# Optimization experiments

Measured on AMD Instinct MI355X. Metric: run time of the kernel, lower is better.

Reference implementation:

```python
import jax, jax.numpy as jnp
import numpy as np

N, NFEAT, NFEAT_EXT, NHID, NCLASS, NHEADS = 8192, 512, 128, 256, 10, 8


def setup_inputs() -> dict:
    key = jax.random.key(0)
    ks = jax.random.split(key, 12)
    s = lambda fan_in: 1.0 / np.sqrt(fan_in)
    return {
        "x": jax.random.normal(ks[0], (N, NFEAT), jnp.float32),
        "adj": jax.random.uniform(ks[1], (N, N), jnp.float32) / N,  # row-stochastic-ish normalized adjacency
        "sub_fea": jax.random.normal(ks[2], (1, NFEAT_EXT), jnp.float32),
        # GraphConvolution 1: nfeat -> nhid
        "gc1_W": jax.random.normal(ks[3], (NFEAT, NHID), jnp.float32) * s(NFEAT),
        "gc1_b": jnp.zeros((NHID,), jnp.float32),
        # GraphConvolution 2: nhid -> 2*nhid
        "gc2_W": jax.random.normal(ks[4], (NHID, 2 * NHID), jnp.float32) * s(NHID),
        "gc2_b": jnp.zeros((2 * NHID,), jnp.float32),
        # fc1: nfeat_ext -> nhid
        "fc1_W": jax.random.normal(ks[5], (NFEAT_EXT, NHID), jnp.float32) * s(NFEAT_EXT),
        "fc1_b": jnp.zeros((NHID,), jnp.float32),
        # AttentionLayer(3*nhid, nclass, nheads): per-head projection + softmax head gating
        "att_W": jax.random.normal(ks[6], (NHEADS, 3 * NHID, NCLASS), jnp.float32) * s(3 * NHID),
        "att_a": jax.random.normal(ks[7], (NHEADS, 3 * NHID), jnp.float32) * s(3 * NHID),
        "att_b": jnp.zeros((NCLASS,), jnp.float32),
    }


def reference(x, adj, sub_fea, gc1_W, gc1_b, gc2_W, gc2_b, fc1_W, fc1_b, att_W, att_a, att_b):
    # GCN layer 1: adj @ (x @ W) + b, then ReLU
    h = jax.nn.relu(adj @ (x @ gc1_W) + gc1_b)            # [N, nhid]
    # GCN layer 2
    h = jax.nn.relu(adj @ (h @ gc2_W) + gc2_b)            # [N, 2*nhid]
    # global_mean_pool(batch=None): mean over all nodes -> single graph vector
    g = jax.nn.selu(jnp.mean(h, axis=0, keepdims=True))    # [1, 2*nhid]
    # dropout is identity in eval mode
    x_ext = sub_fea @ fc1_W + fc1_b                        # [1, nhid]
    z = jnp.concatenate([g, x_ext], axis=1)                # [1, 3*nhid]
    # multi-head attention fusion: softmax over head scores gating per-head projections
    scores = jnp.einsum("bi,hi->bh", z, att_a)            # [1, nheads]
    alpha = jax.nn.softmax(scores, axis=1)
    head_out = jnp.einsum("bi,hio->bho", z, att_W)        # [1, nheads, nclass]
    out = jnp.einsum("bh,bho->bo", alpha, head_out) + att_b  # [1, nclass]
    return jax.nn.log_softmax(out, axis=1)
```

## Files before the change

### kernel.cpp

```cpp
#include <hip/hip_runtime.h>

typedef __attribute__((ext_vector_type(8))) short short8;
typedef __attribute__((ext_vector_type(4))) float floatx4;
typedef unsigned short ushort_t;
typedef unsigned int u32;

__device__ __forceinline__ ushort_t f2bf(float x) {
  union { float f; unsigned int u; } v; v.f = x;
  unsigned int u = v.u;
  return (ushort_t)((u + 0x7FFFu + ((u >> 16) & 1u)) >> 16);
}
__device__ __forceinline__ unsigned int pk2(float a, float b) {
  return (unsigned int)f2bf(a) | ((unsigned int)f2bf(b) << 16);
}
__device__ __forceinline__ float bf_lo(u32 u) {
  union { u32 u; float f; } v; v.u = u << 16; return v.f;
}
__device__ __forceinline__ float bf_hi(u32 u) {
  union { u32 u; float f; } v; v.u = u & 0xFFFF0000u; return v.f;
}
__device__ __forceinline__ void gl_lds16(const void* g, void* l) {
  __builtin_amdgcn_global_load_lds(
      (const __attribute__((address_space(1))) u32*)g,
      (__attribute__((address_space(3))) u32*)l, 16, 0, 0);
}


__global__ void prep_t(const float* __restrict__ W1, const float* __restrict__ W2,
                       ushort_t* __restrict__ W1T, ushort_t* __restrict__ W2T) {
  int idx = blockIdx.x * 256 + threadIdx.x;
  int m = idx >> 9, k = idx & 511;
  W1T[((m >> 7) * 64 + (k >> 3)) * 1024 + (m & 127) * 8 + (k & 7)] = f2bf(W1[k * 256 + m]);
  int m2 = idx >> 8, k2 = idx & 255;
  W2T[((m2 >> 7) * 32 + (k2 >> 3)) * 1024 + (m2 & 127) * 8 + (k2 & 7)] = f2bf(W2[k2 * 512 + m2]);
}

__global__ __launch_bounds__(256) void tile_cvt(const float* __restrict__ src,
                                                ushort_t* __restrict__ dst, const int K) {
  __shared__ __align__(16) ushort_t ls[33024];
  const int t = threadIdx.x;
  const int rb = blockIdx.y, cb = blockIdx.x;
  const long sbase = (long)rb * 128 * K + cb * 256;
#pragma unroll 4
  for (int i = 0; i < 32; ++i) {
    int flat = i * 256 + t;
    int row = flat >> 6, kq = flat & 63;
    float4 v = *(const float4*)(src + sbase + (long)row * K + kq * 4);
    *(uint2*)(ls + ((kq >> 1) * 129 + row) * 8 + (kq & 1) * 4) =
        make_uint2(pk2(v.x, v.y), pk2(v.z, v.w));
  }
  __syncthreads();
  ushort_t* ob = dst + ((long)rb * (K >> 3) + cb * 32) * 1024;
  const uint4* lv = (const uint4*)ls;
  uint4* ov = (uint4*)ob;
#pragma unroll 4
  for (int i = 0; i < 16; ++i) {
    int o = i * 256 + t;
    ov[o] = lv[(o >> 7) * 129 + (o & 127)];
  }
}

template<int MT, int NT, int EPI>
__global__ __launch_bounds__(256, 2)
void gemm_t(const ushort_t* __restrict__ A, const ushort_t* __restrict__ B,
            const float* __restrict__ bias, float* __restrict__ Cf,
            float* __restrict__ gacc, const int K, const int N) {
  constexpr int MF = MT / 32, NF = NT / 32;
  constexpr int nA = MT / 64, nB = NT / 64;
  __shared__ __align__(16) ushort_t Als[2][MT * 32];
  __shared__ __align__(16) ushort_t Bls[2][NT * 32];

  const int t = threadIdx.x;
  const int lane = t & 63, w = t >> 6;
  const int wm = w >> 1, wn = w & 1;
  const int ml = lane & 15, quad = lane >> 4;
  const int m0 = blockIdx.y * MT, n0 = blockIdx.x * NT;
  const int Kper = K / gridDim.z, kbeg = blockIdx.z * Kper;

  const char* Ag = (const char*)(A + ((long)((m0 / MT) * (K >> 3) + (kbeg >> 3)) * MT) * 8);
  const char* Bg = (const char*)(B + ((long)((n0 / NT) * (K >> 3) + (kbeg >> 3)) * NT) * 8);

  floatx4 acc[MF][NF] = {};
  const int iters = Kper >> 5;

#pragma unroll
  for (int c = 0; c < nA; ++c)
    gl_lds16(Ag + c * 4096 + t * 16, (char*)Als[0] + c * 4096 + t * 16);
#pragma unroll
  for (int c = 0; c < nB; ++c)
    gl_lds16(Bg + c * 4096 + t * 16, (char*)Bls[0] + c * 4096 + t * 16);
  Ag += MT * 64; Bg += NT * 64;

  for (int it = 0; it < iters; ++it) {
    const int cur = it & 1, nxt = cur ^ 1;
    __syncthreads();
    if (it + 1 < iters) {
#pragma unroll
      for (int c = 0; c < nA; ++c)
        gl_lds16(Ag + c * 4096 + t * 16, (char*)Als[nxt] + c * 4096 + t * 16);
#pragma unroll
      for (int c = 0; c < nB; ++c)
        gl_lds16(Bg + c * 4096 + t * 16, (char*)Bls[nxt] + c * 4096 + t * 16);
      Ag += MT * 64; Bg += NT * 64;
    }

    short8 av[MF], bv[NF];
#pragma unroll
    for (int f = 0; f < MF; ++f)
      av[f] = *(const short8*)(&Als[cur][0] + (quad * MT + wm * (MT / 2) + f * 16 + ml) * 8);
#pragma unroll
    for (int f = 0; f < NF; ++f)
      bv[f] = *(const short8*)(&Bls[cur][0] + (quad * NT + wn * (NT / 2) + f * 16 + ml) * 8);
#pragma unroll
    for (int fm = 0; fm < MF; ++fm)
#pragma unroll
      for (int fn = 0; fn < NF; ++fn)
        acc[fm][fn] = __builtin_amdgcn_mfma_f32_16x16x32_bf16(av[fm], bv[fn], acc[fm][fn], 0, 0, 0);
  }

  if constexpr (EPI == 2) {
#pragma unroll
    for (int fm = 0; fm < MF; ++fm) {
      int rowb = m0 + wm * (MT / 2) + fm * 16 + quad * 4;
#pragma unroll
      for (int r = 0; r < 4; ++r) {
        float bb = bias[rowb + r];
        float s = 0.f;
#pragma unroll
        for (int fn = 0; fn < NF; ++fn)
          s += fmaxf(acc[fm][fn][r] + bb, 0.f);
        s += __shfl_xor(s, 1);
        s += __shfl_xor(s, 2);
        s += __shfl_xor(s, 4);
        s += __shfl_xor(s, 8);
        if (ml == 0) atomicAdd(gacc + rowb + r, s);
      }
    }
  } else if constexpr (EPI == 3) {
    const int tv = (NT == 256) ? blockIdx.y : blockIdx.x;
    u32* base = (u32*)Cf + ((long)blockIdx.z * 64 + tv) * (MF * NF * 8 * 64)
                + (w * MF * NF * 2) * 64 + lane;
#pragma unroll
    for (int fm = 0; fm < MF; ++fm)
#pragma unroll
      for (int fn = 0; fn < NF; ++fn)
#pragma unroll
        for (int rp = 0; rp < 2; ++rp)
          base[((fm * NF + fn) * 2 + rp) * 64] =
              pk2(acc[fm][fn][2 * rp], acc[fm][fn][2 * rp + 1]);
  } else {
    ushort_t* C = (ushort_t*)Cf;
#pragma unroll
    for (int fm = 0; fm < MF; ++fm)
#pragma unroll
      for (int fn = 0; fn < NF; ++fn) {
        int gm = m0 + wm * (MT / 2) + fm * 16 + quad * 4;
        int gn = n0 + wn * (NT / 2) + fn * 16 + ml;
        long ob = (long)(gn >> 3) * 2048 + (gn & 7);
#pragma unroll
        for (int r = 0; r < 4; ++r)
          C[ob + (long)(gm + r) * 8] = f2bf(acc[fm][fn][r]);
      }
  }
}

__global__ void reduce_L1b(const u32* __restrict__ p, ushort_t* __restrict__ h1T,
                           const float* __restrict__ bias) {
  long i = (long)blockIdx.x * 256 + threadIdx.x;
  long o = i * 4;
  int row = (int)((o >> 3) & 255);
  int k0 = (int)((o >> 11) << 3) + (int)(o & 7);
  int tx = k0 >> 7, c0 = k0 & 127;
  int wm = row >> 7, fm = (row >> 4) & 7, quad = (row >> 2) & 3, r = row & 3;
  int wn = c0 >> 6, fn = (c0 >> 4) & 3, ml = c0 & 15;
  int slot = (((wm * 2 + wn) * 8 + fm) * 4 + fn) * 2 + (r >> 1);
  const u32* src = p + (long)tx * 16384 + slot * 64 + quad * 16 + ml;
  const bool hi = r & 1;
  float s0 = 0, s1 = 0, s2 = 0, s3 = 0;
  for (int z = 0; z < 8; ++z) {
    uint4 v = *(const uint4*)(src + (long)z * 1048576);
    if (hi) { s0 += bf_hi(v.x); s1 += bf_hi(v.y); s2 += bf_hi(v.z); s3 += bf_hi(v.w); }
    else    { s0 += bf_lo(v.x); s1 += bf_lo(v.y); s2 += bf_lo(v.z); s3 += bf_lo(v.w); }
  }
  float bb = bias[row];
  s0 = fmaxf(s0 + bb, 0.f); s1 = fmaxf(s1 + bb, 0.f);
  s2 = fmaxf(s2 + bb, 0.f); s3 = fmaxf(s3 + bb, 0.f);
  *(uint2*)(h1T + o) = make_uint2(pk2(s0, s1), pk2(s2, s3));
}

__global__ void reduce_L2a(const u32* __restrict__ p, ushort_t* __restrict__ P_t) {
  long i = (long)blockIdx.x * 256 + threadIdx.x;
  long o = i * 4;
  int row = (int)((o >> 3) & 127);
  int kc = (int)((o >> 10) & 31);
  int ty = (int)(o >> 15);
  int k0 = kc * 8 + (int)(o & 7);
  int wm = row >> 6, fm = (row >> 4) & 3, quad = (row >> 2) & 3, r = row & 3;
  int wn = k0 >> 7, fn = (k0 >> 4) & 7, ml = k0 & 15;
  int slot = (((wm * 2 + wn) * 4 + fm) * 8 + fn) * 2 + (r >> 1);
  const u32* src = p + (long)ty * 16384 + slot * 64 + quad * 16 + ml;
  const bool hi = r & 1;
  float s0 = 0, s1 = 0, s2 = 0, s3 = 0;
  for (int z = 0; z < 8; ++z) {
    uint4 v = *(const uint4*)(src + (long)z * 1048576);
    if (hi) { s0 += bf_hi(v.x); s1 += bf_hi(v.y); s2 += bf_hi(v.z); s3 += bf_hi(v.w); }
    else    { s0 += bf_lo(v.x); s1 += bf_lo(v.y); s2 += bf_lo(v.z); s3 += bf_lo(v.w); }
  }
  *(uint2*)(P_t + o) = make_uint2(pk2(s0, s1), pk2(s2, s3));
}

__global__ void tail_kernel(const float* __restrict__ gacc, const float* __restrict__ sub_fea,
                            const float* __restrict__ fc1_W, const float* __restrict__ fc1_b,
                            const float* __restrict__ att_W, const float* __restrict__ att_a,
                            const float* __restrict__ att_b, float* __restrict__ out) {
  __shared__ float z[768];
  __shared__ float sc[8];
  __shared__ float alpha[8];
  __shared__ float outsh[10];
  const int t = threadIdx.x;

  for (int j = t; j < 512; j += 256) {
    float x = gacc[j] * (1.0f / 8192.0f);
    const float scale = 1.0507009873554805f, al = 1.6732632423543772f;
    z[j] = x > 0.f ? scale * x : scale * al * (expf(x) - 1.0f);
  }
  {
    float a = fc1_b[t];
    for (int i = 0; i < 128; ++i) a += sub_fea[i] * fc1_W[i * 256 + t];
    z[512 + t] = a;
  }
  if (t < 10) outsh[t] = 0.f;
  __syncthreads();

  {
    int h = t >> 5, ln = t & 31;
    float p = 0.f;
    for (int i = ln; i < 768; i += 32) p += z[i] * att_a[h * 768 + i];
    for (int m = 16; m; m >>= 1) p += __shfl_down(p, m, 32);
    if (ln == 0) sc[h] = p;
  }
  __syncthreads();
  if (t == 0) {
    float mx = sc[0];
    for (int h = 1; h < 8; ++h) mx = fmaxf(mx, sc[h]);
    float s = 0.f, e[8];
    for (int h = 0; h < 8; ++h) { e[h] = expf(sc[h] - mx); s += e[h]; }
    for (int h = 0; h < 8; ++h) alpha[h] = e[h] / s;
  }
  __syncthreads();

  float p[10];
#pragma unroll
  for (int o = 0; o < 10; ++o) p[o] = 0.f;
  for (int i = t; i < 768; i += 256) {
    float zi = z[i];
    for (int h = 0; h < 8; ++h) {
      float za = zi * alpha[h];
      const float* wp = att_W + (h * 768 + i) * 10;
#pragma unroll
      for (int o = 0; o < 10; ++o) p[o] += za * wp[o];
    }
  }
#pragma unroll
  for (int o = 0; o < 10; ++o) atomicAdd(&outsh[o], p[o]);
  __syncthreads();
  if (t == 0) {
    float v[10], mx = -1e30f;
    for (int o = 0; o < 10; ++o) { v[o] = outsh[o] + att_b[o]; mx = fmaxf(mx, v[o]); }
    float s = 0.f;
    for (int o = 0; o < 10; ++o) s += expf(v[o] - mx);
    float lse = logf(s) + mx;
    for (int o = 0; o < 10; ++o) out[o] = v[o] - lse;
  }
}

extern "C" void kernel_launch(void* const* d_in, const int* in_sizes, int n_in,
                              void* d_out, int out_size, void* d_ws, size_t ws_size,
                              hipStream_t stream) {
  const float* x       = (const float*)d_in[0];
  const float* adj     = (const float*)d_in[1];
  const float* sub_fea = (const float*)d_in[2];
  const float* gc1_W   = (const float*)d_in[3];
  const float* gc1_b   = (const float*)d_in[4];
  const float* gc2_W   = (const float*)d_in[5];
  const float* gc2_b   = (const float*)d_in[6];
  const float* fc1_W   = (const float*)d_in[7];
  const float* fc1_b   = (const float*)d_in[8];
  const float* att_W   = (const float*)d_in[9];
  const float* att_a   = (const float*)d_in[10];
  const float* att_b   = (const float*)d_in[11];
  float* out = (float*)d_out;

  const size_t MB = 1u << 20;
  char* ws = (char*)d_ws;
  size_t off = 0;
  ushort_t* adjT = (ushort_t*)(ws + off); off += 128 * MB;
  ushort_t* xT   = (ushort_t*)(ws + off); off += 8 * MB;
  ushort_t* t1T  = (ushort_t*)(ws + off); off += 4 * MB;
  ushort_t* h1T  = (ushort_t*)(ws + off); off += 4 * MB;
  ushort_t* P_t  = (ushort_t*)(ws + off); off += 4 * MB;
  u32*      part = (u32*)     (ws + off); off += 32 * MB;
  ushort_t* W1T  = (ushort_t*)(ws + off); off += 262144;
  ushort_t* W2T  = (ushort_t*)(ws + off); off += 262144;
  float*    gacc = (float*)   (ws + off);

  hipMemsetAsync(gacc, 0, 512 * sizeof(float), stream);
  prep_t<<<512, 256, 0, stream>>>(gc1_W, gc2_W, W1T, W2T);

  tile_cvt<<<dim3(32, 64), 256, 0, stream>>>(adj, adjT, 8192);
  tile_cvt<<<dim3(2, 64), 256, 0, stream>>>(x, xT, 512);

  gemm_t<128, 128, 4><<<dim3(64, 2, 1), 256, 0, stream>>>(
      W1T, xT, nullptr, (float*)t1T, nullptr, 512, 8192);

  gemm_t<256, 128, 3><<<dim3(64, 1, 8), 256, 0, stream>>>(
      t1T, adjT, nullptr, (float*)part, nullptr, 8192, 8192);
  reduce_L1b<<<2048, 256, 0, stream>>>(part, h1T, gc1_b);

  gemm_t<128, 256, 3><<<dim3(1, 64, 8), 256, 0, stream>>>(
      adjT, h1T, nullptr, (float*)part, nullptr, 8192, 256);
  reduce_L2a<<<2048, 256, 0, stream>>>(part, P_t);

  gemm_t<128, 128, 2><<<dim3(64, 4, 1), 256, 0, stream>>>(
      W2T, P_t, gc2_b, nullptr, gacc, 256, 8192);

  tail_kernel<<<1, 256, 0, stream>>>(gacc, sub_fea, fc1_W, fc1_b, att_W, att_a, att_b, out);
}
```

Baseline: 615.6 us.

## Switch adjacency GEMMs to FP8 MFMA with scaled FP8 operands

Converts the adjacency matrix to FP8 (scaled by N) instead of bf16, and stores the t1 and h1 intermediates as FP8 with compensating scales. The two large adjacency GEMMs then use a new FP8 MFMA kernel. This halves the bytes of the dominant adjacency read and conversion write and uses the higher-throughput FP8 matrix path. The cost is lower precision from FP8 rounding, plus scale factors that have to be undone in the reduce kernels.

Result: faster. 588.4 us (-4.4%).

```diff
diff --git a/kernel.cpp b/kernel.cpp
--- a/kernel.cpp
+++ b/kernel.cpp
@@ -4,6 +4,7 @@
 typedef __attribute__((ext_vector_type(4))) float floatx4;
 typedef unsigned short ushort_t;
 typedef unsigned int u32;
+typedef unsigned char u8;
 
 __device__ __forceinline__ ushort_t f2bf(float x) {
   union { float f; unsigned int u; } v; v.f = x;
@@ -18,6 +19,14 @@
 }
 __device__ __forceinline__ float bf_hi(u32 u) {
   union { u32 u; float f; } v; v.u = u & 0xFFFF0000u; return v.f;
+}
+__device__ __forceinline__ u32 pk4_fp8(float a, float b, float c, float d) {
+  int r = __builtin_amdgcn_cvt_pk_fp8_f32(a, b, 0, false);
+  r = __builtin_amdgcn_cvt_pk_fp8_f32(c, d, r, true);
+  return (u32)r;
+}
+__device__ __forceinline__ u8 f2fp8(float a) {
+  return (u8)(__builtin_amdgcn_cvt_pk_fp8_f32(a, 0.f, 0, false) & 0xFF);
 }
 __device__ __forceinline__ void gl_lds16(const void* g, void* l) {
   __builtin_amdgcn_global_load_lds(
@@ -60,10 +69,35 @@
   }
 }
 
+__global__ __launch_bounds__(256) void tile_cvt8(const float* __restrict__ src,
+                                                 u8* __restrict__ dst) {
+  __shared__ __align__(16) u32 lsu[32 * 260];
+  const int t = threadIdx.x;
+  const int rb = blockIdx.y, cb = blockIdx.x;
+  const long sbase = (long)rb * 128 * 8192 + cb * 256;
+#pragma unroll 4
+  for (int i = 0; i < 32; ++i) {
+    int flat = i * 256 + t;
+    int row = flat >> 6, kq = flat & 63;
+    float4 v = *(const float4*)(src + sbase + (long)row * 8192 + kq * 4);
+    lsu[(kq >> 1) * 260 + row * 2 + (kq & 1)] =
+        pk4_fp8(v.x * 8192.f, v.y * 8192.f, v.z * 8192.f, v.w * 8192.f);
+  }
+  __syncthreads();
+  u8* ob = dst + ((long)rb * 1024 + cb * 32) * 1024;
+  const uint4* lv = (const uint4*)lsu;
+  uint4* ov = (uint4*)ob;
+#pragma unroll 4
+  for (int i = 0; i < 8; ++i) {
+    int o = i * 256 + t;
+    ov[o] = lv[(o >> 6) * 65 + (o & 63)];
+  }
+}
+
 template<int MT, int NT, int EPI>
 __global__ __launch_bounds__(256, 2)
 void gemm_t(const ushort_t* __restrict__ A, const ushort_t* __restrict__ B,
-            const float* __restrict__ bias, float* __restrict__ Cf,
+            const float* __restrict__ bias, void* __restrict__ Cv,
             float* __restrict__ gacc, const int K, const int N) {
   constexpr int MF = MT / 32, NF = NT / 32;
   constexpr int nA = MT / 64, nB = NT / 64;
@@ -103,7 +137,6 @@
         gl_lds16(Bg + c * 4096 + t * 16, (char*)Bls[nxt] + c * 4096 + t * 16);
       Ag += MT * 64; Bg += NT * 64;
     }
-
     short8 av[MF], bv[NF];
 #pragma unroll
     for (int f = 0; f < MF; ++f)
@@ -136,20 +169,8 @@
         if (ml == 0) atomicAdd(gacc + rowb + r, s);
       }
     }
-  } else if constexpr (EPI == 3) {
-    const int tv = (NT == 256) ? blockIdx.y : blockIdx.x;
-    u32* base = (u32*)Cf + ((long)blockIdx.z * 64 + tv) * (MF * NF * 8 * 64)
-                + (w * MF * NF * 2) * 64 + lane;
-#pragma unroll
-    for (int fm = 0; fm < MF; ++fm)
-#pragma unroll
-      for (int fn = 0; fn < NF; ++fn)
-#pragma unroll
-        for (int rp = 0; rp < 2; ++rp)
-          base[((fm * NF + fn) * 2 + rp) * 64] =
-              pk2(acc[fm][fn][2 * rp], acc[fm][fn][2 * rp + 1]);
   } else {
-    ushort_t* C = (ushort_t*)Cf;
+    u8* C8 = (u8*)Cv;
 #pragma unroll
     for (int fm = 0; fm < MF; ++fm)
 #pragma unroll
@@ -159,12 +180,81 @@
         long ob = (long)(gn >> 3) * 2048 + (gn & 7);
 #pragma unroll
         for (int r = 0; r < 4; ++r)
-          C[ob + (long)(gm + r) * 8] = f2bf(acc[fm][fn][r]);
+          C8[ob + (long)(gm + r) * 8] = f2fp8(acc[fm][fn][r]);
       }
   }
 }
 
-__global__ void reduce_L1b(const u32* __restrict__ p, ushort_t* __restrict__ h1T,
+template<int MT, int NT>
+__global__ __launch_bounds__(256, 2)
+void gemm8_t(const u8* __restrict__ A, const u8* __restrict__ B,
+             u32* __restrict__ Cp, const int K) {
+  constexpr int MF = MT / 32, NF = NT / 32;
+  constexpr int nA = MT / 128, nB = NT / 128;
+  __shared__ __align__(16) u8 Als[2][MT * 32];
+  __shared__ __align__(16) u8 Bls[2][NT * 32];
+
+  const int t = threadIdx.x;
+  const int lane = t & 63, w = t >> 6;
+  const int wm = w >> 1, wn = w & 1;
+  const int ml = lane & 15, quad = lane >> 4;
+  const int m0 = blockIdx.y * MT, n0 = blockIdx.x * NT;
+  const int Kper = K / gridDim.z, kbeg = blockIdx.z * Kper;
+
+  const u8* Ag = A + ((long)((m0 / MT) * (K >> 3) + (kbeg >> 3))) * (MT * 8);
+  const u8* Bg = B + ((long)((n0 / NT) * (K >> 3) + (kbeg >> 3))) * (NT * 8);
+
+  floatx4 acc[MF][NF] = {};
+  const int iters = Kper >> 5;
+
+#pragma unroll
+  for (int c = 0; c < nA; ++c)
+    gl_lds16(Ag + c * 4096 + t * 16, &Als[0][0] + c * 4096 + t * 16);
+#pragma unroll
+  for (int c = 0; c < nB; ++c)
+    gl_lds16(Bg + c * 4096 + t * 16, &Bls[0][0] + c * 4096 + t * 16);
+  Ag += MT * 32; Bg += NT * 32;
+
+  for (int it = 0; it < iters; ++it) {
+    const int cur = it & 1, nxt = cur ^ 1;
+    __syncthreads();
+    if (it + 1 < iters) {
+#pragma unroll
+      for (int c = 0; c < nA; ++c)
+        gl_lds16(Ag + c * 4096 + t * 16, &Als[nxt][0] + c * 4096 + t * 16);
+#pragma unroll
+      for (int c = 0; c < nB; ++c)
+        gl_lds16(Bg + c * 4096 + t * 16, &Bls[nxt][0] + c * 4096 + t * 16);
+      Ag += MT * 32; Bg += NT * 32;
+    }
+    long av[MF], bv[NF];
+#pragma unroll
+    for (int f = 0; f < MF; ++f)
+      av[f] = *(const long*)(&Als[cur][0] + (quad * MT + wm * (MT / 2) + f * 16 + ml) * 8);
+#pragma unroll
+    for (int f = 0; f < NF; ++f)
+      bv[f] = *(const long*)(&Bls[cur][0] + (quad * NT + wn * (NT / 2) + f * 16 + ml) * 8);
+#pragma unroll
+    for (int fm = 0; fm < MF; ++fm)
+#pragma unroll
+      for (int fn = 0; fn < NF; ++fn)
+        acc[fm][fn] = __builtin_amdgcn_mfma_f32_16x16x32_fp8_fp8(av[fm], bv[fn], acc[fm][fn], 0, 0, 0);
+  }
+
+  const int tv = (NT == 256) ? blockIdx.y : blockIdx.x;
+  u32* base = Cp + ((long)blockIdx.z * 64 + tv) * (MF * NF * 8 * 64)
+              + (w * MF * NF * 2) * 64 + lane;
+#pragma unroll
+  for (int fm = 0; fm < MF; ++fm)
+#pragma unroll
+    for (int fn = 0; fn < NF; ++fn)
+#pragma unroll
+      for (int rp = 0; rp < 2; ++rp)
+        base[((fm * NF + fn) * 2 + rp) * 64] =
+            pk2(acc[fm][fn][2 * rp], acc[fm][fn][2 * rp + 1]);
+}
+
+__global__ void reduce_L1b(const u32* __restrict__ p, u8* __restrict__ h1T8,
                            const float* __restrict__ bias) {
   long i = (long)blockIdx.x * 256 + threadIdx.x;
   long o = i * 4;
@@ -182,10 +272,11 @@
     if (hi) { s0 += bf_hi(v.x); s1 += bf_hi(v.y); s2 += bf_hi(v.z); s3 += bf_hi(v.w); }
     else    { s0 += bf_lo(v.x); s1 += bf_lo(v.y); s2 += bf_lo(v.z); s3 += bf_lo(v.w); }
   }
+  const float si = 1.f / 8192.f, so = 256.f;
   float bb = bias[row];
-  s0 = fmaxf(s0 + bb, 0.f); s1 = fmaxf(s1 + bb, 0.f);
-  s2 = fmaxf(s2 + bb, 0.f); s3 = fmaxf(s3 + bb, 0.f);
-  *(uint2*)(h1T + o) = make_uint2(pk2(s0, s1), pk2(s2, s3));
+  s0 = fmaxf(s0 * si + bb, 0.f) * so; s1 = fmaxf(s1 * si + bb, 0.f) * so;
+  s2 = fmaxf(s2 * si + bb, 0.f) * so; s3 = fmaxf(s3 * si + bb, 0.f) * so;
+  *(u32*)(h1T8 + o) = pk4_fp8(s0, s1, s2, s3);
 }
 
 __global__ void reduce_L2a(const u32* __restrict__ p, ushort_t* __restrict__ P_t) {
@@ -206,7 +297,8 @@
     if (hi) { s0 += bf_hi(v.x); s1 += bf_hi(v.y); s2 += bf_hi(v.z); s3 += bf_hi(v.w); }
     else    { s0 += bf_lo(v.x); s1 += bf_lo(v.y); s2 += bf_lo(v.z); s3 += bf_lo(v.w); }
   }
-  *(uint2*)(P_t + o) = make_uint2(pk2(s0, s1), pk2(s2, s3));
+  const float sc = 1.f / 2097152.f;
+  *(uint2*)(P_t + o) = make_uint2(pk2(s0 * sc, s1 * sc), pk2(s2 * sc, s3 * sc));
 }
 
 __global__ void tail_kernel(const float* __restrict__ gacc, const float* __restrict__ sub_fea,
@@ -294,31 +386,29 @@
   const size_t MB = 1u << 20;
   char* ws = (char*)d_ws;
   size_t off = 0;
-  ushort_t* adjT = (ushort_t*)(ws + off); off += 128 * MB;
-  ushort_t* xT   = (ushort_t*)(ws + off); off += 8 * MB;
-  ushort_t* t1T  = (ushort_t*)(ws + off); off += 4 * MB;
-  ushort_t* h1T  = (ushort_t*)(ws + off); off += 4 * MB;
-  ushort_t* P_t  = (ushort_t*)(ws + off); off += 4 * MB;
-  u32*      part = (u32*)     (ws + off); off += 32 * MB;
-  ushort_t* W1T  = (ushort_t*)(ws + off); off += 262144;
-  ushort_t* W2T  = (ushort_t*)(ws + off); off += 262144;
-  float*    gacc = (float*)   (ws + off);
+  u8*       adjT8 = (u8*)      (ws + off); off += 64 * MB;
+  ushort_t* xT    = (ushort_t*)(ws + off); off += 8 * MB;
+  u8*       t1T8  = (u8*)      (ws + off); off += 2 * MB;
+  u8*       h1T8  = (u8*)      (ws + off); off += 2 * MB;
+  ushort_t* P_t   = (ushort_t*)(ws + off); off += 4 * MB;
+  u32*      part  = (u32*)     (ws + off); off += 32 * MB;
+  ushort_t* W1T   = (ushort_t*)(ws + off); off += 262144;
+  ushort_t* W2T   = (ushort_t*)(ws + off); off += 262144;
+  float*    gacc  = (float*)   (ws + off);
 
   hipMemsetAsync(gacc, 0, 512 * sizeof(float), stream);
   prep_t<<<512, 256, 0, stream>>>(gc1_W, gc2_W, W1T, W2T);
-
-  tile_cvt<<<dim3(32, 64), 256, 0, stream>>>(adj, adjT, 8192);
   tile_cvt<<<dim3(2, 64), 256, 0, stream>>>(x, xT, 512);
 
-  gemm_t<128, 128, 4><<<dim3(64, 2, 1), 256, 0, stream>>>(
-      W1T, xT, nullptr, (float*)t1T, nullptr, 512, 8192);
-
-  gemm_t<256, 128, 3><<<dim3(64, 1, 8), 256, 0, stream>>>(
-      t1T, adjT, nullptr, (float*)part, nullptr, 8192, 8192);
-  reduce_L1b<<<2048, 256, 0, stream>>>(part, h1T, gc1_b);
-
-  gemm_t<128, 256, 3><<<dim3(1, 64, 8), 256, 0, stream>>>(
-      adjT, h1T, nullptr, (float*)part, nullptr, 8192, 256);
+  gemm_t<128, 128, 5><<<dim3(64, 2, 1), 256, 0, stream>>>(
+      W1T, xT, nullptr, t1T8, nullptr, 512, 8192);
+
+  tile_cvt8<<<dim3(32, 64), 256, 0, stream>>>(adj, adjT8);
+
+  gemm8_t<256, 128><<<dim3(64, 1, 8), 256, 0, stream>>>(t1T8, adjT8, part, 8192);
+  reduce_L1b<<<2048, 256, 0, stream>>>(part, h1T8, gc1_b);
+
+  gemm8_t<128, 256><<<dim3(1, 64, 8), 256, 0, stream>>>(adjT8, h1T8, part, 8192);
   reduce_L2a<<<2048, 256, 0, stream>>>(part, P_t);
 
   gemm_t<128, 128, 2><<<dim3(64, 4, 1), 256, 0, stream>>>(
```
